# Performance work log

Measured on AMD Instinct MI355X. Metric: run time of the kernel, lower is better.

Reference implementation:

```python
import jax, jax.numpy as jnp
import numpy as np

B, S, D_IN, D_OUT, H = 2, 2048, 1024, 1024, 16
HD = D_OUT // H


def setup_inputs() -> dict:
    key = jax.random.key(0)
    ks = jax.random.split(key, 6)
    s_in = 1.0 / np.sqrt(D_IN)
    s_out = 1.0 / np.sqrt(D_OUT)
    return {
        "x": jax.random.normal(ks[0], (B, S, D_IN), dtype=jnp.float32),
        "wq": jax.random.uniform(ks[1], (D_IN, D_OUT), jnp.float32, -s_in, s_in),
        "wk": jax.random.uniform(ks[2], (D_IN, D_OUT), jnp.float32, -s_in, s_in),
        "wv": jax.random.uniform(ks[3], (D_IN, D_OUT), jnp.float32, -s_in, s_in),
        "wo": jax.random.uniform(ks[4], (D_OUT, D_OUT), jnp.float32, -s_out, s_out),
        "bo": jax.random.uniform(ks[5], (D_OUT,), jnp.float32, -s_out, s_out),
    }


def reference(x, wq, wk, wv, wo, bo):
    # QKV projections (qkv_bias=False)
    q = (x @ wq).reshape(B, S, H, HD)  # [B,S,H,hd]
    k = (x @ wk).reshape(B, S, H, HD)
    v = (x @ wv).reshape(B, S, H, HD)
    # scores [B,H,S,S], scaled by sqrt(head_dim)
    scores = jnp.einsum("bqhd,bkhd->bhqk", q, k) / np.sqrt(HD).astype(np.float32)
    attn = jax.nn.softmax(scores, axis=-1)  # dropout=0.0 -> no-op
    ctx = jnp.einsum("bhqk,bkhd->bqhd", attn, v).reshape(B, S, D_OUT)
    return ctx @ wo + bo
```

## Files before the change

kernel.cpp:

```cpp
#include <hip/hip_runtime.h>
#include <stdint.h>


typedef __attribute__((ext_vector_type(8))) short bf16x8;
typedef __attribute__((ext_vector_type(4))) float f32x4;

__device__ __forceinline__ unsigned short f2bf(float f) {
  unsigned u = __builtin_bit_cast(unsigned, f);
  u = (u + 0x7fffu + ((u >> 16) & 1u)) >> 16;
  return (unsigned short)u;
}
__device__ __forceinline__ float bf2f(unsigned short h) {
  unsigned u = ((unsigned)h) << 16;
  return __builtin_bit_cast(float, u);
}
__device__ __forceinline__ f32x4 mfma16(bf16x8 a, bf16x8 b, f32x4 c) {
  return __builtin_amdgcn_mfma_f32_16x16x32_bf16(a, b, c, 0, 0, 0);
}

__global__ __launch_bounds__(256) void cast_x_kernel(const float* __restrict__ x,
                                                     unsigned short* __restrict__ xb) {
  long i = (long)blockIdx.x * 256 + threadIdx.x;
  const float4* p = (const float4*)x + i * 2;
  float4 a = p[0], b = p[1];
  union { unsigned short us[8]; uint4 v; } o;
  o.us[0] = f2bf(a.x); o.us[1] = f2bf(a.y); o.us[2] = f2bf(a.z); o.us[3] = f2bf(a.w);
  o.us[4] = f2bf(b.x); o.us[5] = f2bf(b.y); o.us[6] = f2bf(b.z); o.us[7] = f2bf(b.w);
  ((uint4*)xb)[i] = o.v;
}

template<bool SPLIT>
__global__ __launch_bounds__(256) void transpose_cast_kernel(const float* __restrict__ w,
                                                             unsigned short* __restrict__ hi,
                                                             unsigned short* __restrict__ lo) {
  __shared__ float t[32][33];
  int tid = threadIdx.x;
  int c = tid & 31, rr = tid >> 5;
  int k0 = blockIdx.x * 32, n0 = blockIdx.y * 32;
#pragma unroll
  for (int i = 0; i < 4; i++) t[rr + i * 8][c] = w[(size_t)(k0 + rr + i * 8) * 1024 + n0 + c];
  __syncthreads();
#pragma unroll
  for (int i = 0; i < 4; i++) {
    float v = t[c][rr + i * 8];
    size_t o = (size_t)(n0 + rr + i * 8) * 1024 + k0 + c;
    unsigned short hv = f2bf(v);
    hi[o] = hv;
    if (SPLIT) lo[o] = f2bf(v - bf2f(hv));
  }
}

__device__ __forceinline__ void stage_tile64(const unsigned short* src, unsigned short* lds,
                                             int wid, int lane) {
#pragma unroll
  for (int c4 = 0; c4 < 4; ++c4) {
    int c = wid * 4 + c4;
    int row = c * 8 + (lane >> 3);
    int colb = ((lane & 7) * 16) ^ ((row & 7) << 4);
    const unsigned short* gp = src + (size_t)row * 1024 + (colb >> 1);
    __builtin_amdgcn_global_load_lds((const __attribute__((address_space(1))) void*)gp,
                                     (__attribute__((address_space(3))) void*)(lds + c * 512),
                                     16, 0, 0);
  }
}
template<int SRC_STRIDE>
__device__ __forceinline__ void stage64(const unsigned short* src, unsigned short* lds,
                                        int wid, int lane) {
#pragma unroll
  for (int c4 = 0; c4 < 2; ++c4) {
    int c = wid * 2 + c4;
    int row = c * 8 + (lane >> 3);
    int colb = ((lane & 7) * 16) ^ ((row & 7) << 4);
    const unsigned short* gp = src + (size_t)row * SRC_STRIDE + (colb >> 1);
    __builtin_amdgcn_global_load_lds((const __attribute__((address_space(1))) void*)gp,
                                     (__attribute__((address_space(3))) void*)(lds + c * 512),
                                     16, 0, 0);
  }
}
__device__ __forceinline__ bf16x8 frag_ld(const unsigned short* lds, int row, int kbyte) {
  int colb = kbyte ^ ((row & 7) << 4);
  return *(const bf16x8*)((const char*)lds + row * 128 + colb);
}

__global__ __launch_bounds__(256) void gemm_qkv_kernel(const unsigned short* __restrict__ xb,
    const unsigned short* __restrict__ wqT, const unsigned short* __restrict__ wkT,
    const unsigned short* __restrict__ wvT,
    unsigned short* __restrict__ qb, unsigned short* __restrict__ kb,
    unsigned short* __restrict__ vtb) {
  __shared__ unsigned short AS[128 * 64];
  __shared__ unsigned short BS[128 * 64];
  int tid = threadIdx.x, lane = tid & 63, wid = tid >> 6;
  int g = lane >> 4, cl = lane & 15;
  int m0 = blockIdx.x * 128, n0 = blockIdx.y * 128;
  int z = blockIdx.z;
  const unsigned short* wT = (z == 0) ? wqT : (z == 1) ? wkT : wvT;
  int wm = wid >> 1, wn = wid & 1;
  f32x4 acc[4][4] = {};
  for (int kt = 0; kt < 16; ++kt) {
    stage_tile64(xb + (size_t)m0 * 1024 + kt * 64, AS, wid, lane);
    stage_tile64(wT + (size_t)n0 * 1024 + kt * 64, BS, wid, lane);
    __syncthreads();
#pragma unroll
    for (int kk = 0; kk < 2; ++kk) {
      bf16x8 af[4], bfr[4];
#pragma unroll
      for (int i = 0; i < 4; ++i) af[i] = frag_ld(AS, wm * 64 + i * 16 + cl, kk * 64 + g * 16);
#pragma unroll
      for (int i = 0; i < 4; ++i) bfr[i] = frag_ld(BS, wn * 64 + i * 16 + cl, kk * 64 + g * 16);
#pragma unroll
      for (int m = 0; m < 4; ++m)
#pragma unroll
        for (int n = 0; n < 4; ++n)
          acc[m][n] = mfma16(af[m], bfr[n], acc[m][n]);
    }
    __syncthreads();
  }
#pragma unroll
  for (int m = 0; m < 4; ++m)
#pragma unroll
    for (int n = 0; n < 4; ++n) {
      int nn = n0 + wn * 64 + n * 16 + cl;
#pragma unroll
      for (int r = 0; r < 4; ++r) {
        int mm = m0 + wm * 64 + m * 16 + g * 4 + r;
        unsigned short val = f2bf(acc[m][n][r]);
        size_t bh = (size_t)((mm >> 11) * 16 + (nn >> 6));
        if (z < 2) {
          unsigned short* dst = (z == 0) ? qb : kb;
          dst[bh * 131072 + (size_t)(mm & 2047) * 64 + (nn & 63)] = val;
        } else {
          vtb[bh * 131072 + (size_t)(nn & 63) * 2048 + (mm & 2047)] = val;
        }
      }
    }
}

__global__ __launch_bounds__(256) void attn_kernel(const unsigned short* __restrict__ qb,
                                                   const unsigned short* __restrict__ kb,
                                                   const unsigned short* __restrict__ vtb,
                                                   unsigned short* __restrict__ ch,
                                                   unsigned short* __restrict__ clo) {
  __shared__ unsigned short Ksm[2][64 * 64];
  __shared__ unsigned short Vsm[2][64 * 64];
  __shared__ unsigned short Psm[4][32 * 72];
  int tid = threadIdx.x, lane = tid & 63, wid = tid >> 6;
  int g = lane >> 4, cl = lane & 15;
  int lin = blockIdx.x + (blockIdx.y << 4);
  int swz = (lin & 7) * 64 + (lin >> 3);
  int bh = swz >> 4;
  int q0 = (swz & 15) * 128 + wid * 32;
  size_t base = (size_t)bh * 131072;

  bf16x8 qf[2][2];
#pragma unroll
  for (int mf = 0; mf < 2; ++mf)
#pragma unroll
    for (int kk = 0; kk < 2; ++kk)
      qf[mf][kk] = *(const bf16x8*)(qb + base + (size_t)(q0 + mf * 16 + cl) * 64 + kk * 32 + g * 8);

  bf16x8 onesv;
#pragma unroll
  for (int i = 0; i < 8; ++i) onesv[i] = (short)0x3F80;

  f32x4 accO[2][4] = {};
  f32x4 accL[2] = {};

  stage64<64>(kb + base, &Ksm[0][0], wid, lane);
  stage64<2048>(vtb + base, &Vsm[0][0], wid, lane);
  __syncthreads();

  int cur = 0;
  for (int t = 0; t < 32; ++t) {
    if (t < 31) {
      stage64<64>(kb + base + (size_t)(t + 1) * 4096, &Ksm[cur ^ 1][0], wid, lane);
      stage64<2048>(vtb + base + (size_t)(t + 1) * 64, &Vsm[cur ^ 1][0], wid, lane);
    }

    f32x4 s[2][4] = {};
#pragma unroll
    for (int kk = 0; kk < 2; ++kk) {
      bf16x8 kf[4];
#pragma unroll
      for (int nf = 0; nf < 4; ++nf)
        kf[nf] = frag_ld(&Ksm[cur][0], nf * 16 + cl, kk * 64 + g * 16);
#pragma unroll
      for (int mf = 0; mf < 2; ++mf)
#pragma unroll
        for (int nf = 0; nf < 4; ++nf)
          s[mf][nf] = mfma16(qf[mf][kk], kf[nf], s[mf][nf]);
    }

#pragma unroll
    for (int mf = 0; mf < 2; ++mf)
#pragma unroll
      for (int r = 0; r < 4; ++r) {
        int qrow = mf * 16 + g * 4 + r;
#pragma unroll
        for (int nf = 0; nf < 4; ++nf) {
          float p = __builtin_amdgcn_exp2f(fmaf(s[mf][nf][r], 0.18033688011112042f, -8.0f));
          Psm[wid][qrow * 72 + nf * 16 + cl] = f2bf(p);
        }
      }
    __builtin_amdgcn_sched_barrier(0);

#pragma unroll
    for (int kk = 0; kk < 2; ++kk) {
      bf16x8 pa[2], vb[4];
#pragma unroll
      for (int mf = 0; mf < 2; ++mf)
        pa[mf] = *(const bf16x8*)&Psm[wid][(mf * 16 + cl) * 72 + kk * 32 + g * 8];
#pragma unroll
      for (int nf = 0; nf < 4; ++nf)
        vb[nf] = frag_ld(&Vsm[cur][0], nf * 16 + cl, kk * 64 + g * 16);
#pragma unroll
      for (int mf = 0; mf < 2; ++mf) {
#pragma unroll
        for (int nf = 0; nf < 4; ++nf)
          accO[mf][nf] = mfma16(pa[mf], vb[nf], accO[mf][nf]);
        accL[mf] = mfma16(pa[mf], onesv, accL[mf]);
      }
    }
    __syncthreads();
    cur ^= 1;
  }

  int b = bh >> 4, h = bh & 15;
#pragma unroll
  for (int mf = 0; mf < 2; ++mf)
#pragma unroll
    for (int r = 0; r < 4; ++r) {
      float inv = 1.0f / accL[mf][r];
      int qg = q0 + mf * 16 + g * 4 + r;
      size_t rowb = ((size_t)(b * 2048 + qg)) * 1024 + h * 64;
#pragma unroll
      for (int nf = 0; nf < 4; ++nf) {
        float o = accO[mf][nf][r] * inv;
        int d = nf * 16 + cl;
        unsigned short hv = f2bf(o);
        ch[rowb + d] = hv;
        clo[rowb + d] = f2bf(o - bf2f(hv));
      }
    }
}

__global__ __launch_bounds__(256) void gemm_out_kernel(const unsigned short* __restrict__ cah,
    const unsigned short* __restrict__ cal, const unsigned short* __restrict__ wbh,
    const unsigned short* __restrict__ wbl, const float* __restrict__ bias,
    float* __restrict__ out) {
  __shared__ unsigned short AhS[128 * 64], AlS[128 * 64], BhS[128 * 64], BlS[128 * 64];
  int tid = threadIdx.x, lane = tid & 63, wid = tid >> 6;
  int g = lane >> 4, cl = lane & 15;
  int m0 = blockIdx.x * 128, n0 = blockIdx.y * 128;
  int wm = wid >> 1, wn = wid & 1;
  f32x4 acc[4][4] = {};
  for (int kt = 0; kt < 16; ++kt) {
    stage_tile64(cah + (size_t)m0 * 1024 + kt * 64, AhS, wid, lane);
    stage_tile64(cal + (size_t)m0 * 1024 + kt * 64, AlS, wid, lane);
    stage_tile64(wbh + (size_t)n0 * 1024 + kt * 64, BhS, wid, lane);
    stage_tile64(wbl + (size_t)n0 * 1024 + kt * 64, BlS, wid, lane);
    __syncthreads();
#pragma unroll
    for (int kk = 0; kk < 2; ++kk) {
      bf16x8 ah[4], al[4], bh[4], bl[4];
#pragma unroll
      for (int i = 0; i < 4; ++i) {
        ah[i] = frag_ld(AhS, wm * 64 + i * 16 + cl, kk * 64 + g * 16);
        al[i] = frag_ld(AlS, wm * 64 + i * 16 + cl, kk * 64 + g * 16);
        bh[i] = frag_ld(BhS, wn * 64 + i * 16 + cl, kk * 64 + g * 16);
        bl[i] = frag_ld(BlS, wn * 64 + i * 16 + cl, kk * 64 + g * 16);
      }
#pragma unroll
      for (int m = 0; m < 4; ++m)
#pragma unroll
        for (int n = 0; n < 4; ++n) {
          acc[m][n] = mfma16(ah[m], bh[n], acc[m][n]);
          acc[m][n] = mfma16(ah[m], bl[n], acc[m][n]);
          acc[m][n] = mfma16(al[m], bh[n], acc[m][n]);
        }
    }
    __syncthreads();
  }
#pragma unroll
  for (int n = 0; n < 4; ++n) {
    int nn = n0 + wn * 64 + n * 16 + cl;
    float bv = bias[nn];
#pragma unroll
    for (int m = 0; m < 4; ++m)
#pragma unroll
      for (int r = 0; r < 4; ++r) {
        int mm = m0 + wm * 64 + m * 16 + g * 4 + r;
        out[(size_t)mm * 1024 + nn] = acc[m][n][r] + bv;
      }
  }
}

extern "C" void kernel_launch(void* const* d_in, const int* in_sizes, int n_in,
                              void* d_out, int out_size, void* d_ws, size_t ws_size,
                              hipStream_t stream) {
  (void)in_sizes; (void)n_in; (void)out_size; (void)ws_size;
  const float* x  = (const float*)d_in[0];
  const float* wq = (const float*)d_in[1];
  const float* wk = (const float*)d_in[2];
  const float* wv = (const float*)d_in[3];
  const float* wo = (const float*)d_in[4];
  const float* bo = (const float*)d_in[5];
  float* out = (float*)d_out;

  char* ws = (char*)d_ws;
  unsigned short* xb   = (unsigned short*)(ws);
  unsigned short* wqT  = (unsigned short*)(ws + (8ull  << 20));
  unsigned short* wkT  = (unsigned short*)(ws + (10ull << 20));
  unsigned short* wvT  = (unsigned short*)(ws + (12ull << 20));
  unsigned short* woTh = (unsigned short*)(ws + (14ull << 20));
  unsigned short* woTl = (unsigned short*)(ws + (16ull << 20));
  unsigned short* qb   = (unsigned short*)(ws + (18ull << 20));
  unsigned short* kb   = (unsigned short*)(ws + (26ull << 20));
  unsigned short* vtb  = (unsigned short*)(ws + (34ull << 20));
  unsigned short* ch   = (unsigned short*)(ws + (42ull << 20));
  unsigned short* clo  = (unsigned short*)(ws + (50ull << 20));

  cast_x_kernel<<<2048, 256, 0, stream>>>(x, xb);
  transpose_cast_kernel<false><<<dim3(32, 32), 256, 0, stream>>>(wq, wqT, nullptr);
  transpose_cast_kernel<false><<<dim3(32, 32), 256, 0, stream>>>(wk, wkT, nullptr);
  transpose_cast_kernel<false><<<dim3(32, 32), 256, 0, stream>>>(wv, wvT, nullptr);
  transpose_cast_kernel<true ><<<dim3(32, 32), 256, 0, stream>>>(wo, woTh, woTl);
  gemm_qkv_kernel<<<dim3(32, 8, 3), 256, 0, stream>>>(xb, wqT, wkT, wvT, qb, kb, vtb);
  attn_kernel<<<dim3(16, 32), 256, 0, stream>>>(qb, kb, vtb, ch, clo);
  gemm_out_kernel<<<dim3(32, 8), 256, 0, stream>>>(ch, clo, woTh, woTl, bo, out);
}
```

Baseline: 227.6 us.

## Merge QKV weight transposes, swizzle GEMM block order, add MFMA priority hints, shrink out-GEMM tile

```diff
diff --git a/kernel.cpp b/kernel.cpp
--- a/kernel.cpp
+++ b/kernel.cpp
@@ -29,10 +29,27 @@
   ((uint4*)xb)[i] = o.v;
 }
 
-template<bool SPLIT>
-__global__ __launch_bounds__(256) void transpose_cast_kernel(const float* __restrict__ w,
-                                                             unsigned short* __restrict__ hi,
-                                                             unsigned short* __restrict__ lo) {
+__global__ __launch_bounds__(256) void transpose_qkv_kernel(const float* __restrict__ wq,
+    const float* __restrict__ wk, const float* __restrict__ wv,
+    unsigned short* __restrict__ wqT, unsigned short* __restrict__ wkT,
+    unsigned short* __restrict__ wvT) {
+  const float* w = (blockIdx.z == 0) ? wq : (blockIdx.z == 1) ? wk : wv;
+  unsigned short* o = (blockIdx.z == 0) ? wqT : (blockIdx.z == 1) ? wkT : wvT;
+  __shared__ float t[32][33];
+  int tid = threadIdx.x;
+  int c = tid & 31, rr = tid >> 5;
+  int k0 = blockIdx.x * 32, n0 = blockIdx.y * 32;
+#pragma unroll
+  for (int i = 0; i < 4; i++) t[rr + i * 8][c] = w[(size_t)(k0 + rr + i * 8) * 1024 + n0 + c];
+  __syncthreads();
+#pragma unroll
+  for (int i = 0; i < 4; i++)
+    o[(size_t)(n0 + rr + i * 8) * 1024 + k0 + c] = f2bf(t[c][rr + i * 8]);
+}
+
+__global__ __launch_bounds__(256) void transpose_wo_kernel(const float* __restrict__ w,
+                                                           unsigned short* __restrict__ hi,
+                                                           unsigned short* __restrict__ lo) {
   __shared__ float t[32][33];
   int tid = threadIdx.x;
   int c = tid & 31, rr = tid >> 5;
@@ -46,7 +63,7 @@
     size_t o = (size_t)(n0 + rr + i * 8) * 1024 + k0 + c;
     unsigned short hv = f2bf(v);
     hi[o] = hv;
-    if (SPLIT) lo[o] = f2bf(v - bf2f(hv));
+    lo[o] = f2bf(v - bf2f(hv));
   }
 }
 
@@ -91,8 +108,10 @@
   __shared__ unsigned short BS[128 * 64];
   int tid = threadIdx.x, lane = tid & 63, wid = tid >> 6;
   int g = lane >> 4, cl = lane & 15;
-  int m0 = blockIdx.x * 128, n0 = blockIdx.y * 128;
-  int z = blockIdx.z;
+  int lin = blockIdx.x + (blockIdx.y << 5) + (blockIdx.z << 8);
+  int swz = (lin & 7) * 96 + (lin >> 3);
+  int z = swz >> 8, rem = swz & 255;
+  int m0 = (rem & 31) * 128, n0 = (rem >> 5) * 128;
   const unsigned short* wT = (z == 0) ? wqT : (z == 1) ? wkT : wvT;
   int wm = wid >> 1, wn = wid & 1;
   f32x4 acc[4][4] = {};
@@ -107,11 +126,13 @@
       for (int i = 0; i < 4; ++i) af[i] = frag_ld(AS, wm * 64 + i * 16 + cl, kk * 64 + g * 16);
 #pragma unroll
       for (int i = 0; i < 4; ++i) bfr[i] = frag_ld(BS, wn * 64 + i * 16 + cl, kk * 64 + g * 16);
+      __builtin_amdgcn_s_setprio(1);
 #pragma unroll
       for (int m = 0; m < 4; ++m)
 #pragma unroll
         for (int n = 0; n < 4; ++n)
           acc[m][n] = mfma16(af[m], bfr[n], acc[m][n]);
+      __builtin_amdgcn_s_setprio(0);
     }
     __syncthreads();
   }
@@ -183,11 +204,13 @@
 #pragma unroll
       for (int nf = 0; nf < 4; ++nf)
         kf[nf] = frag_ld(&Ksm[cur][0], nf * 16 + cl, kk * 64 + g * 16);
+      __builtin_amdgcn_s_setprio(1);
 #pragma unroll
       for (int mf = 0; mf < 2; ++mf)
 #pragma unroll
         for (int nf = 0; nf < 4; ++nf)
           s[mf][nf] = mfma16(qf[mf][kk], kf[nf], s[mf][nf]);
+      __builtin_amdgcn_s_setprio(0);
     }
 
 #pragma unroll
@@ -212,6 +235,7 @@
 #pragma unroll
       for (int nf = 0; nf < 4; ++nf)
         vb[nf] = frag_ld(&Vsm[cur][0], nf * 16 + cl, kk * 64 + g * 16);
+      __builtin_amdgcn_s_setprio(1);
 #pragma unroll
       for (int mf = 0; mf < 2; ++mf) {
 #pragma unroll
@@ -219,6 +243,7 @@
           accO[mf][nf] = mfma16(pa[mf], vb[nf], accO[mf][nf]);
         accL[mf] = mfma16(pa[mf], onesv, accL[mf]);
       }
+      __builtin_amdgcn_s_setprio(0);
     }
     __syncthreads();
     cur ^= 1;
@@ -247,48 +272,55 @@
     const unsigned short* __restrict__ cal, const unsigned short* __restrict__ wbh,
     const unsigned short* __restrict__ wbl, const float* __restrict__ bias,
     float* __restrict__ out) {
-  __shared__ unsigned short AhS[128 * 64], AlS[128 * 64], BhS[128 * 64], BlS[128 * 64];
+  __shared__ unsigned short AhS[64 * 64], AlS[64 * 64];
+  __shared__ unsigned short BhS[128 * 64], BlS[128 * 64];
   int tid = threadIdx.x, lane = tid & 63, wid = tid >> 6;
   int g = lane >> 4, cl = lane & 15;
-  int m0 = blockIdx.x * 128, n0 = blockIdx.y * 128;
-  int wm = wid >> 1, wn = wid & 1;
-  f32x4 acc[4][4] = {};
+  int lin = blockIdx.x + (blockIdx.y << 6);
+  int swz = (lin & 7) * 64 + (lin >> 3);
+  int m0 = (swz & 63) * 64, n0 = (swz >> 6) * 128;
+  f32x4 acc[4][2] = {};
   for (int kt = 0; kt < 16; ++kt) {
-    stage_tile64(cah + (size_t)m0 * 1024 + kt * 64, AhS, wid, lane);
-    stage_tile64(cal + (size_t)m0 * 1024 + kt * 64, AlS, wid, lane);
+    stage64<1024>(cah + (size_t)m0 * 1024 + kt * 64, AhS, wid, lane);
+    stage64<1024>(cal + (size_t)m0 * 1024 + kt * 64, AlS, wid, lane);
     stage_tile64(wbh + (size_t)n0 * 1024 + kt * 64, BhS, wid, lane);
     stage_tile64(wbl + (size_t)n0 * 1024 + kt * 64, BlS, wid, lane);
     __syncthreads();
 #pragma unroll
     for (int kk = 0; kk < 2; ++kk) {
-      bf16x8 ah[4], al[4], bh[4], bl[4];
+      bf16x8 ah[4], al[4], bh[2], bl[2];
 #pragma unroll
       for (int i = 0; i < 4; ++i) {
-        ah[i] = frag_ld(AhS, wm * 64 + i * 16 + cl, kk * 64 + g * 16);
-        al[i] = frag_ld(AlS, wm * 64 + i * 16 + cl, kk * 64 + g * 16);
-        bh[i] = frag_ld(BhS, wn * 64 + i * 16 + cl, kk * 64 + g * 16);
-        bl[i] = frag_ld(BlS, wn * 64 + i * 16 + cl, kk * 64 + g * 16);
-      }
+        ah[i] = frag_ld(AhS, i * 16 + cl, kk * 64 + g * 16);
+        al[i] = frag_ld(AlS, i * 16 + cl, kk * 64 + g * 16);
+      }
+#pragma unroll
+      for (int i = 0; i < 2; ++i) {
+        bh[i] = frag_ld(BhS, wid * 32 + i * 16 + cl, kk * 64 + g * 16);
+        bl[i] = frag_ld(BlS, wid * 32 + i * 16 + cl, kk * 64 + g * 16);
+      }
+      __builtin_amdgcn_s_setprio(1);
 #pragma unroll
       for (int m = 0; m < 4; ++m)
 #pragma unroll
-        for (int n = 0; n < 4; ++n) {
+        for (int n = 0; n < 2; ++n) {
           acc[m][n] = mfma16(ah[m], bh[n], acc[m][n]);
           acc[m][n] = mfma16(ah[m], bl[n], acc[m][n]);
           acc[m][n] = mfma16(al[m], bh[n], acc[m][n]);
         }
-    }
-    __syncthreads();
-  }
-#pragma unroll
-  for (int n = 0; n < 4; ++n) {
-    int nn = n0 + wn * 64 + n * 16 + cl;
+      __builtin_amdgcn_s_setprio(0);
+    }
+    __syncthreads();
+  }
+#pragma unroll
+  for (int n = 0; n < 2; ++n) {
+    int nn = n0 + wid * 32 + n * 16 + cl;
     float bv = bias[nn];
 #pragma unroll
     for (int m = 0; m < 4; ++m)
 #pragma unroll
       for (int r = 0; r < 4; ++r) {
-        int mm = m0 + wm * 64 + m * 16 + g * 4 + r;
+        int mm = m0 + m * 16 + g * 4 + r;
         out[(size_t)mm * 1024 + nn] = acc[m][n][r] + bv;
       }
   }
@@ -320,11 +352,9 @@
   unsigned short* clo  = (unsigned short*)(ws + (50ull << 20));
 
   cast_x_kernel<<<2048, 256, 0, stream>>>(x, xb);
-  transpose_cast_kernel<false><<<dim3(32, 32), 256, 0, stream>>>(wq, wqT, nullptr);
-  transpose_cast_kernel<false><<<dim3(32, 32), 256, 0, stream>>>(wk, wkT, nullptr);
-  transpose_cast_kernel<false><<<dim3(32, 32), 256, 0, stream>>>(wv, wvT, nullptr);
-  transpose_cast_kernel<true ><<<dim3(32, 32), 256, 0, stream>>>(wo, woTh, woTl);
+  transpose_qkv_kernel<<<dim3(32, 32, 3), 256, 0, stream>>>(wq, wk, wv, wqT, wkT, wvT);
+  transpose_wo_kernel<<<dim3(32, 32), 256, 0, stream>>>(wo, woTh, woTl);
   gemm_qkv_kernel<<<dim3(32, 8, 3), 256, 0, stream>>>(xb, wqT, wkT, wvT, qb, kb, vtb);
   attn_kernel<<<dim3(16, 32), 256, 0, stream>>>(qb, kb, vtb, ch, clo);
-  gemm_out_kernel<<<dim3(32, 8), 256, 0, stream>>>(ch, clo, woTh, woTl, bo, out);
-}
+  gemm_out_kernel<<<dim3(64, 8), 256, 0, stream>>>(ch, clo, woTh, woTl, bo, out);
+}
```

After: 225.7 us. Within noise of the previous version (-0.8%).
